# Performance work log

Measured on AMD Instinct MI355X. Metric: run time of the kernel, lower is better.

The kernel has to match this reference:

```python
import jax, jax.numpy as jnp
import numpy as np


def _conv(x, w, pad, groups=1):
    # NCHW conv, OIHW weights, stride 1
    return jax.lax.conv_general_dilated(
        x, w, (1, 1), [(pad, pad), (pad, pad)],
        dimension_numbers=('NCHW', 'OIHW', 'NCHW'),
        feature_group_count=groups)


def setup_inputs() -> dict:
    key = jax.random.key(0)
    ks = jax.random.split(key, 16)
    b, c, h, w = 4, 64, 256, 256
    heads = 8
    s = 0.05
    inp = {
        'x': jax.random.normal(ks[0], (b, c, h, w), jnp.float32),
        # qkv 1x1 conv (with bias) then depthwise 3x3 (with bias)
        'w_qkv': jax.random.normal(ks[1], (3 * c, c, 1, 1), jnp.float32) * s,
        'b_qkv': jax.random.normal(ks[2], (3 * c,), jnp.float32) * s,
        'w_dw': jax.random.normal(ks[3], (3 * c, 1, 3, 3), jnp.float32) * s,
        'b_dw': jax.random.normal(ks[4], (3 * c,), jnp.float32) * s,
        # project_out 1x1 (with bias)
        'w_proj': jax.random.normal(ks[5], (c, c, 1, 1), jnp.float32) * s,
        'b_proj': jax.random.normal(ks[6], (c,), jnp.float32) * s,
        'temperature': jnp.ones((heads, 1, 1), jnp.float32),
        # V_MaskAttention.conv2: 1x1(no bias) -> BN -> 5x5 pad2(no bias)
        'w_m1': jax.random.normal(ks[7], (c, c, 1, 1), jnp.float32) * s,
        'bn_gamma': jnp.ones((c,), jnp.float32),
        'bn_beta': jnp.zeros((c,), jnp.float32),
        'bn_mean': jax.random.normal(ks[8], (c,), jnp.float32) * 0.1,
        'bn_var': jax.random.uniform(ks[9], (c,), jnp.float32, 0.5, 1.5),
        'w_m2': jax.random.normal(ks[10], (c, c, 5, 5), jnp.float32) * s,
    }
    return inp


def reference(x, w_qkv, b_qkv, w_dw, b_dw, w_proj, b_proj, temperature,
              w_m1, bn_gamma, bn_beta, bn_mean, bn_var, w_m2):
    b, c, h, w = x.shape
    heads = temperature.shape[0]

    # qkv conv1x1 + depthwise 3x3 (v chunk computed but unused, as in source)
    qkv = _conv(x, w_qkv, 0) + b_qkv[None, :, None, None]
    qkv = _conv(qkv, w_dw, 1, groups=3 * c) + b_dw[None, :, None, None]
    q, k, _ = jnp.split(qkv, 3, axis=1)

    # V_MaskAttention gated value path (BN in eval mode, eps=1e-5)
    y = _conv(x, w_m1, 0)
    y = (y - bn_mean[None, :, None, None]) * (
        bn_gamma[None, :, None, None]
        / jnp.sqrt(bn_var[None, :, None, None] + 1e-5)) + bn_beta[None, :, None, None]
    x2 = jax.nn.sigmoid(_conv(y, w_m2, 2))
    v = x + x * x2

    def heads_view(t):  # b,(head c),h,w -> b,head,c_head,hw
        return t.reshape(b, heads, c // heads, h * w)

    q = heads_view(q)
    k = heads_view(k)
    v = heads_view(v)

    # L2 normalize over spatial dim (torch F.normalize eps=1e-12)
    q = q / jnp.maximum(jnp.linalg.norm(q, axis=-1, keepdims=True), 1e-12)
    k = k / jnp.maximum(jnp.linalg.norm(k, axis=-1, keepdims=True), 1e-12)

    attn = jnp.einsum('bhcn,bhdn->bhcd', q, k) * temperature[None]  # [b,h,c',c']
    attn = jax.nn.softmax(attn, axis=-1)
    out = jnp.einsum('bhcd,bhdn->bhcn', attn, v).reshape(b, c, h, w)
    return _conv(out, w_proj, 0) + b_proj[None, :, None, None]
```

## Files before the change

kernel.cpp:

```cpp
#include <hip/hip_runtime.h>
#include <math.h>

#define B 4
#define C 64
#define NN 65536

typedef __attribute__((ext_vector_type(8))) short short8;
typedef __attribute__((ext_vector_type(4))) short short4b;
typedef __attribute__((ext_vector_type(4))) float f32x4;
typedef __attribute__((ext_vector_type(4))) unsigned int u32x4;

__device__ inline float bf2f(short s) {
  union { unsigned u; float f; } v; v.u = ((unsigned)(unsigned short)s) << 16; return v.f;
}
__device__ inline short f2bf(float f) {
  union { float f; unsigned u; } v; v.f = f;
  unsigned r = v.u + 0x7FFFu + ((v.u >> 16) & 1u);
  return (short)(r >> 16);
}
__device__ inline float lof(unsigned u) {
  union { unsigned u; float f; } v; v.u = u << 16; return v.f;
}
__device__ inline float hif(unsigned u) {
  union { unsigned u; float f; } v; v.u = u & 0xffff0000u; return v.f;
}

__global__ void k_prep1(const float* __restrict__ wqkv, const float* __restrict__ wm1,
    short* __restrict__ apk, short* __restrict__ apm, float* __restrict__ gram2) {
  for (int idx = blockIdx.x * 256 + threadIdx.x; idx < 20480; idx += 16384) {
    if (idx < 8192) {
      const int j = idx & 7, lane = (idx >> 3) & 63, mt = (idx >> 9) & 7, cc = idx >> 12;
      const int o = mt * 16 + (lane & 15), c = cc * 32 + (lane >> 4) * 8 + j;
      apk[idx] = f2bf(wqkv[o * 64 + c]);
    } else if (idx < 12288) {
      const int k = idx - 8192;
      const int j = k & 7, lane = (k >> 3) & 63, mt = (k >> 9) & 3, cc = k >> 11;
      const int o = mt * 16 + (lane & 15), c = cc * 32 + (lane >> 4) * 8 + j;
      apm[k] = f2bf(wm1[o * 64 + c]);
    } else {
      gram2[idx - 12288] = 0.f;
    }
  }
}

__global__ void k_prep2(const float* __restrict__ w2, short* __restrict__ apw2) {
  for (int idx = blockIdx.x * 256 + threadIdx.x; idx < 25 * 2 * 4 * 64 * 8; idx += 16384) {
    const int j = idx & 7, lane = (idx >> 3) & 63, mt = (idx >> 9) & 3,
              cc = (idx >> 11) & 1, t = idx >> 12;
    const int o = mt * 16 + (lane & 15);
    const int c = cc * 32 + (lane >> 4) * 8 + j;
    apw2[idx] = f2bf(w2[((size_t)o * 64 + c) * 25 + t]);
  }
}

__global__ __launch_bounds__(256) void k_xt(const float* __restrict__ x,
    short* __restrict__ x_t) {
  __shared__ short lds[256 * 72];
  const int b = blockIdx.x >> 8, n0 = (blockIdx.x & 255) << 8;
  const int t = threadIdx.x;
#pragma unroll 4
  for (int c = 0; c < 64; ++c)
    lds[t * 72 + c] = f2bf(x[((size_t)(b * 64 + c)) * NN + n0 + t]);
  __syncthreads();
  short* dst = x_t + ((size_t)(b * NN + n0)) * 64;
#pragma unroll
  for (int it = 0; it < 8; ++it) {
    const int idx = it * 256 + t;
    const int nl = idx >> 3, cb = idx & 7;
    *(short8*)(dst + (size_t)nl * 64 + cb * 8) = *(const short8*)(lds + nl * 72 + cb * 8);
  }
}

__global__ __launch_bounds__(256, 4) void k_qk1x1(const short* __restrict__ x_t,
    const short* __restrict__ apk, const float* __restrict__ bias,
    short* __restrict__ qk) {
  const int b = blockIdx.x >> 10, ntile = blockIdx.x & 1023;
  const int wave = threadIdx.x >> 6, lane = threadIdx.x & 63;
  const int quad = lane >> 4, l15 = lane & 15;
  const int n = ntile * 64 + wave * 16 + l15;
  f32x4 acc[8];
#pragma unroll
  for (int mt = 0; mt < 8; ++mt) acc[mt] = (f32x4){0.f, 0.f, 0.f, 0.f};
#pragma unroll
  for (int cc = 0; cc < 2; ++cc) {
    const short8 bf = *(const short8*)(x_t + ((size_t)(b * NN + n)) * 64 + cc * 32 + quad * 8);
#pragma unroll
    for (int mt = 0; mt < 8; ++mt) {
      const short8 af = *(const short8*)(apk + ((cc * 8 + mt) * 64 + lane) * 8);
      acc[mt] = __builtin_amdgcn_mfma_f32_16x16x32_bf16(af, bf, acc[mt], 0, 0, 0);
    }
  }
#pragma unroll
  for (int mt = 0; mt < 8; ++mt)
#pragma unroll
    for (int reg = 0; reg < 4; ++reg) {
      const int o = mt * 16 + quad * 4 + reg;
      qk[((size_t)(b * 128 + o)) * NN + n] = f2bf(acc[mt][reg] + bias[o]);
    }
}

__global__ __launch_bounds__(256, 3) void k_gram(const short* __restrict__ qk,
    const float* __restrict__ wdw, const float* __restrict__ bdw,
    float* __restrict__ gram2) {
  __shared__ float red[4][256];
  const int bh = blockIdx.x >> 6, chunk = blockIdx.x & 63;
  const int b = bh >> 3, h = bh & 7;
  const int wave = threadIdx.x >> 6, lane = threadIdx.x & 63;
  const int quad = lane >> 4, l15 = lane & 15;
  const int ch = (l15 < 8) ? (h * 8 + l15) : (64 + h * 8 + (l15 - 8));
  const short* plane = qk + ((size_t)(b * 128 + ch)) * NN;
  float wreg[9];
#pragma unroll
  for (int i = 0; i < 9; ++i) wreg[i] = wdw[ch * 9 + i];
  const float bias = bdw[ch];
  const int row = chunk * 4 + wave;
  const short* prow = plane + row * 256;
  u32x4 rb[3][8];
#pragma unroll
  for (int dy = 0; dy < 3; ++dy) {
    if (dy == 0 && row == 0) continue;
    if (dy == 2 && row == 255) continue;
    const short* pr = prow + (dy - 1) * 256 + quad * 8;
#pragma unroll
    for (int s = 0; s < 8; ++s)
      rb[dy][s] = *(const u32x4*)(pr + s * 32);
  }
  f32x4 acc = {0.f, 0.f, 0.f, 0.f};
#pragma unroll
  for (int s = 0; s < 8; ++s) {
    float a[8];
#pragma unroll
    for (int j = 0; j < 8; ++j) a[j] = bias;
#pragma unroll
    for (int dy = 0; dy < 3; ++dy) {
      if (dy == 0 && row == 0) continue;
      if (dy == 2 && row == 255) continue;
      const unsigned w0_ = rb[dy][s][0], w1_ = rb[dy][s][1],
                     w2_ = rb[dy][s][2], w3_ = rb[dy][s][3];
      float m[10];
      m[1] = lof(w0_); m[2] = hif(w0_);
      m[3] = lof(w1_); m[4] = hif(w1_);
      m[5] = lof(w2_); m[6] = hif(w2_);
      m[7] = lof(w3_); m[8] = hif(w3_);
      const unsigned A3 = (unsigned)__shfl((int)w3_, (lane - 16) & 63, 64);
      const unsigned A0 = (unsigned)__shfl((int)w0_, (lane + 16) & 63, 64);
      float m0q0 = 0.f, m9q3 = 0.f;
      if (s > 0) {
        const unsigned B3 = (unsigned)__shfl((int)rb[dy][s - 1][3], (lane + 48) & 63, 64);
        m0q0 = hif(B3);
      }
      if (s < 7) {
        const unsigned B0 = (unsigned)__shfl((int)rb[dy][s + 1][0], (lane - 48) & 63, 64);
        m9q3 = lof(B0);
      }
      m[0] = (quad == 0) ? m0q0 : hif(A3);
      m[9] = (quad == 3) ? m9q3 : lof(A0);
      const float W0 = wreg[dy * 3], W1 = wreg[dy * 3 + 1], W2 = wreg[dy * 3 + 2];
#pragma unroll
      for (int j = 0; j < 8; ++j)
        a[j] = fmaf(W2, m[j + 2], fmaf(W1, m[j + 1], fmaf(W0, m[j], a[j])));
    }
    short8 frag;
#pragma unroll
    for (int j = 0; j < 8; ++j) frag[j] = f2bf(a[j]);
    acc = __builtin_amdgcn_mfma_f32_16x16x32_bf16(frag, frag, acc, 0, 0, 0);
  }
#pragma unroll
  for (int reg = 0; reg < 4; ++reg)
    red[wave][(quad * 4 + reg) * 16 + l15] = acc[reg];
  __syncthreads();
  {
    const int e = threadIdx.x;
    const float s4 = red[0][e] + red[1][e] + red[2][e] + red[3][e];
    atomicAdd(&gram2[bh * 256 + e], s4);
  }
}

__global__ __launch_bounds__(256, 4) void k_m1_bn(const short* __restrict__ x_t,
    const short* __restrict__ apm, const float* __restrict__ gamma,
    const float* __restrict__ beta, const float* __restrict__ mean,
    const float* __restrict__ var, short* __restrict__ y_t) {
  __shared__ short lds[64 * 72];
  const int b = blockIdx.x >> 10, ntile = blockIdx.x & 1023;
  const int wave = threadIdx.x >> 6, lane = threadIdx.x & 63;
  const int quad = lane >> 4, l15 = lane & 15;
  const int n = ntile * 64 + wave * 16 + l15;
  f32x4 acc[4];
#pragma unroll
  for (int mt = 0; mt < 4; ++mt) acc[mt] = (f32x4){0.f, 0.f, 0.f, 0.f};
#pragma unroll
  for (int cc = 0; cc < 2; ++cc) {
    const short8 bf = *(const short8*)(x_t + ((size_t)(b * NN + n)) * 64 + cc * 32 + quad * 8);
#pragma unroll
    for (int mt = 0; mt < 4; ++mt) {
      const short8 af = *(const short8*)(apm + ((cc * 4 + mt) * 64 + lane) * 8);
      acc[mt] = __builtin_amdgcn_mfma_f32_16x16x32_bf16(af, bf, acc[mt], 0, 0, 0);
    }
  }
#pragma unroll
  for (int mt = 0; mt < 4; ++mt)
#pragma unroll
    for (int reg = 0; reg < 4; ++reg) {
      const int o = mt * 16 + quad * 4 + reg;
      const float sc = gamma[o] * rsqrtf(var[o] + 1e-5f);
      lds[(wave * 16 + l15) * 72 + o] = f2bf((acc[mt][reg] - mean[o]) * sc + beta[o]);
    }
  __syncthreads();
  short* dst = y_t + ((size_t)(b * NN + ntile * 64)) * 64;
#pragma unroll
  for (int it = 0; it < 2; ++it) {
    const int idx = it * 256 + threadIdx.x;
    const int lcol = idx >> 3, cb = idx & 7;
    *(short8*)(dst + (size_t)lcol * 64 + cb * 8) = *(const short8*)(lds + lcol * 72 + cb * 8);
  }
}

__global__ __launch_bounds__(256, 2) void k_conv5(const short* __restrict__ y_t,
    const short* __restrict__ apw2, const short* __restrict__ x_t,
    short* __restrict__ v_t) {
  __shared__ short slds[4 * 64 * 76];
  char* sb = (char*)slds;
  const int b = blockIdx.x >> 8;
  const int rg = (blockIdx.x >> 2) & 63, cg = blockIdx.x & 3;
  const int r0 = rg * 4, x0 = cg * 64;
  const int wave = threadIdx.x >> 6, lane = threadIdx.x & 63;
  const int quad = lane >> 4, l15 = lane & 15;
  f32x4 acc[4][4];
#pragma unroll
  for (int mt = 0; mt < 4; ++mt)
#pragma unroll
    for (int nt = 0; nt < 4; ++nt) acc[mt][nt] = (f32x4){0.f, 0.f, 0.f, 0.f};
  for (int cc = 0; cc < 2; ++cc) {
    if (cc) __syncthreads();
    for (int idx = threadIdx.x; idx < 8 * 68 * 4; idx += 256) {
      const int rr = idx / 272, rem = idx - rr * 272;
      const int col = rem >> 2, cb = rem & 3;
      const int gr = r0 - 2 + rr, gc = x0 - 2 + col;
      short8 val = {0, 0, 0, 0, 0, 0, 0, 0};
      if (gr >= 0 && gr < 256 && gc >= 0 && gc < 256)
        val = *(const short8*)(y_t + ((size_t)(b * NN + gr * 256 + gc)) * 64 + cc * 32 + cb * 8);
      const int L = rr * 68 + col;
      *(short8*)(sb + ((L * 64 + cb * 16) ^ (((L >> 1) & 3) << 4))) = val;
    }
    __syncthreads();
    for (int t = 0; t < 25; ++t) {
      const int dy = t / 5 - 2, dx = t % 5 - 2;
      short8 a[4];
#pragma unroll
      for (int mt = 0; mt < 4; ++mt)
        a[mt] = *(const short8*)(apw2 + (((t * 2 + cc) * 4 + mt) * 64 + lane) * 8);
      const int rr = wave + 2 + dy;
#pragma unroll
      for (int nt = 0; nt < 4; ++nt) {
        const int L = rr * 68 + nt * 16 + l15 + 2 + dx;
        const short8 bf =
            *(const short8*)(sb + ((L * 64 + quad * 16) ^ (((L >> 1) & 3) << 4)));
#pragma unroll
        for (int mt = 0; mt < 4; ++mt)
          acc[mt][nt] = __builtin_amdgcn_mfma_f32_16x16x32_bf16(a[mt], bf, acc[mt][nt], 0, 0, 0);
      }
    }
  }
  __syncthreads();
  const int row = r0 + wave;
#pragma unroll
  for (int nt = 0; nt < 4; ++nt) {
    const int lcol = nt * 16 + l15;
    const short* xp = x_t + ((size_t)(b * NN + row * 256 + x0 + lcol)) * 64 + quad * 4;
#pragma unroll
    for (int mt = 0; mt < 4; ++mt) {
      const short4b xv4 = *(const short4b*)(xp + mt * 16);
      short4b pk;
#pragma unroll
      for (int reg = 0; reg < 4; ++reg) {
        const float sg = 1.f / (1.f + __expf(-acc[mt][nt][reg]));
        pk[reg] = f2bf(bf2f(xv4[reg]) * (1.f + sg));
      }
      *(short4b*)(slds + (wave * 64 + lcol) * 76 + mt * 16 + quad * 4) = pk;
    }
  }
  __syncthreads();
#pragma unroll
  for (int it = 0; it < 8; ++it) {
    const int idx = it * 256 + threadIdx.x;
    const int cb = idx & 7, lcol = (idx >> 3) & 63, rr = idx >> 9;
    *(short8*)(v_t + ((size_t)(b * NN + (r0 + rr) * 256 + x0 + lcol)) * 64 + cb * 8) =
        *(const short8*)(slds + (rr * 64 + lcol) * 76 + cb * 8);
  }
}

__global__ __launch_bounds__(256) void k_attn_e(const float* __restrict__ gram2,
    const float* __restrict__ temp, const float* __restrict__ wproj,
    short* __restrict__ Epack) {
  __shared__ float attn[2048];
  const int t = threadIdx.x;
  {
    const int b = t >> 6, h = (t >> 3) & 7, c = t & 7;
    const float* g = gram2 + (b * 8 + h) * 256;
    const float qn = fmaxf(sqrtf(g[c * 16 + c]), 1e-12f);
    const float tp = temp[h];
    float row[8];
    float mx = -1e30f;
#pragma unroll
    for (int d = 0; d < 8; ++d) {
      const float kn = fmaxf(sqrtf(g[(8 + d) * 16 + (8 + d)]), 1e-12f);
      row[d] = g[c * 16 + 8 + d] / (qn * kn) * tp;
      mx = fmaxf(mx, row[d]);
    }
    float s = 0.f;
#pragma unroll
    for (int d = 0; d < 8; ++d) { row[d] = __expf(row[d] - mx); s += row[d]; }
    const float inv = 1.f / s;
#pragma unroll
    for (int d = 0; d < 8; ++d) attn[t * 8 + d] = row[d] * inv;
  }
  __syncthreads();
  for (int idx = t; idx < 16384; idx += 256) {
    const int j = idx & 7, lane = (idx >> 3) & 63, mt = (idx >> 9) & 3,
              cc = (idx >> 11) & 1, b = idx >> 12;
    const int o = mt * 16 + (lane & 15);
    const int cv = cc * 32 + (lane >> 4) * 8 + j;
    const int h = cv >> 3, d = cv & 7;
    float a = 0.f;
#pragma unroll
    for (int c2 = 0; c2 < 8; ++c2)
      a += wproj[o * 64 + h * 8 + c2] * attn[((b * 8 + h) * 8 + c2) * 8 + d];
    Epack[idx] = f2bf(a);
  }
}

__global__ __launch_bounds__(256, 4) void k_out(const short* __restrict__ v_t,
    const short* __restrict__ Epack, const float* __restrict__ bproj,
    float* __restrict__ out) {
  const int b = blockIdx.x >> 10, ntile = blockIdx.x & 1023;
  const int wave = threadIdx.x >> 6, lane = threadIdx.x & 63;
  const int quad = lane >> 4, l15 = lane & 15;
  const int n = ntile * 64 + wave * 16 + l15;
  f32x4 acc[4];
#pragma unroll
  for (int mt = 0; mt < 4; ++mt) acc[mt] = (f32x4){0.f, 0.f, 0.f, 0.f};
#pragma unroll
  for (int cc = 0; cc < 2; ++cc) {
    const short8 bf = *(const short8*)(v_t + ((size_t)(b * NN + n)) * 64 + cc * 32 + quad * 8);
#pragma unroll
    for (int mt = 0; mt < 4; ++mt) {
      const short8 af = *(const short8*)(Epack + (((b * 2 + cc) * 4 + mt) * 64 + lane) * 8);
      acc[mt] = __builtin_amdgcn_mfma_f32_16x16x32_bf16(af, bf, acc[mt], 0, 0, 0);
    }
  }
#pragma unroll
  for (int mt = 0; mt < 4; ++mt)
#pragma unroll
    for (int reg = 0; reg < 4; ++reg) {
      const int o = mt * 16 + quad * 4 + reg;
      out[((size_t)(b * 64 + o)) * NN + n] = acc[mt][reg] + bproj[o];
    }
}

extern "C" void kernel_launch(void* const* d_in, const int* in_sizes, int n_in,
                              void* d_out, int out_size, void* d_ws, size_t ws_size,
                              hipStream_t stream) {
  const float* x     = (const float*)d_in[0];
  const float* wqkv  = (const float*)d_in[1];
  const float* bqkv  = (const float*)d_in[2];
  const float* wdw   = (const float*)d_in[3];
  const float* bdw   = (const float*)d_in[4];
  const float* wproj = (const float*)d_in[5];
  const float* bproj = (const float*)d_in[6];
  const float* temp  = (const float*)d_in[7];
  const float* wm1   = (const float*)d_in[8];
  const float* gamma = (const float*)d_in[9];
  const float* beta  = (const float*)d_in[10];
  const float* mean  = (const float*)d_in[11];
  const float* var   = (const float*)d_in[12];
  const float* wm2   = (const float*)d_in[13];

  char* wsb = (char*)d_ws;
  short* qk    = (short*)(wsb);
  short* v_t   = (short*)(wsb);
  short* apw2  = (short*)(wsb + 33554432);
  short* x_t   = (short*)(wsb + 67108864);
  short* y_t   = (short*)(wsb + 100663296);
  float* gram2 = (float*)(wsb + 134217728);
  short* apk   = (short*)(wsb + 134217728 + 32768);
  short* apm   = (short*)(wsb + 134217728 + 49152);
  short* Epack = (short*)(wsb + 134217728 + 57344);
  float* out   = (float*)d_out;

  k_prep1<<<dim3(64), dim3(256), 0, stream>>>(wqkv, wm1, apk, apm, gram2);
  k_xt<<<dim3(1024), dim3(256), 0, stream>>>(x, x_t);
  k_qk1x1<<<dim3(4096), dim3(256), 0, stream>>>(x_t, apk, bqkv, qk);
  k_gram<<<dim3(2048), dim3(256), 0, stream>>>(qk, wdw, bdw, gram2);
  k_prep2<<<dim3(64), dim3(256), 0, stream>>>(wm2, apw2);
  k_m1_bn<<<dim3(4096), dim3(256), 0, stream>>>(x_t, apm, gamma, beta, mean, var, y_t);
  k_conv5<<<dim3(1024), dim3(256), 0, stream>>>(y_t, apw2, x_t, v_t);
  k_attn_e<<<dim3(1), dim3(256), 0, stream>>>(gram2, temp, wproj, Epack);
  k_out<<<dim3(4096), dim3(256), 0, stream>>>(v_t, Epack, bproj, out);
}
```

Measured before the change: 308.1 us.

## Fold weight prep into main kernels, single-pass conv5 staging, parallelize attn_e

Result: faster. 299.0 us (-3.0%).

```diff
diff --git a/kernel.cpp b/kernel.cpp
--- a/kernel.cpp
+++ b/kernel.cpp
@@ -25,49 +25,41 @@
   union { unsigned u; float f; } v; v.u = u & 0xffff0000u; return v.f;
 }
 
-__global__ void k_prep1(const float* __restrict__ wqkv, const float* __restrict__ wm1,
-    short* __restrict__ apk, short* __restrict__ apm, float* __restrict__ gram2) {
-  for (int idx = blockIdx.x * 256 + threadIdx.x; idx < 20480; idx += 16384) {
-    if (idx < 8192) {
-      const int j = idx & 7, lane = (idx >> 3) & 63, mt = (idx >> 9) & 7, cc = idx >> 12;
-      const int o = mt * 16 + (lane & 15), c = cc * 32 + (lane >> 4) * 8 + j;
-      apk[idx] = f2bf(wqkv[o * 64 + c]);
-    } else if (idx < 12288) {
-      const int k = idx - 8192;
-      const int j = k & 7, lane = (k >> 3) & 63, mt = (k >> 9) & 3, cc = k >> 11;
-      const int o = mt * 16 + (lane & 15), c = cc * 32 + (lane >> 4) * 8 + j;
-      apm[k] = f2bf(wm1[o * 64 + c]);
-    } else {
-      gram2[idx - 12288] = 0.f;
-    }
-  }
-}
-
-__global__ void k_prep2(const float* __restrict__ w2, short* __restrict__ apw2) {
-  for (int idx = blockIdx.x * 256 + threadIdx.x; idx < 25 * 2 * 4 * 64 * 8; idx += 16384) {
-    const int j = idx & 7, lane = (idx >> 3) & 63, mt = (idx >> 9) & 3,
-              cc = (idx >> 11) & 1, t = idx >> 12;
-    const int o = mt * 16 + (lane & 15);
-    const int c = cc * 32 + (lane >> 4) * 8 + j;
-    apw2[idx] = f2bf(w2[((size_t)o * 64 + c) * 25 + t]);
-  }
-}
-
 __global__ __launch_bounds__(256) void k_xt(const float* __restrict__ x,
-    short* __restrict__ x_t) {
-  __shared__ short lds[256 * 72];
+    short* __restrict__ x_t, const float* __restrict__ wqkv,
+    const float* __restrict__ wm1, short* __restrict__ apk,
+    short* __restrict__ apm, float* __restrict__ gram2) {
+  if (blockIdx.x >= 1024) {
+    const int bid = blockIdx.x - 1024;
+    for (int idx = bid * 256 + threadIdx.x; idx < 20480; idx += 16384) {
+      if (idx < 8192) {
+        const int j = idx & 7, lane = (idx >> 3) & 63, mt = (idx >> 9) & 7, cc = idx >> 12;
+        const int o = mt * 16 + (lane & 15), c = cc * 32 + (lane >> 4) * 8 + j;
+        apk[idx] = f2bf(wqkv[o * 64 + c]);
+      } else if (idx < 12288) {
+        const int k = idx - 8192;
+        const int j = k & 7, lane = (k >> 3) & 63, mt = (k >> 9) & 3, cc = k >> 11;
+        const int o = mt * 16 + (lane & 15), c = cc * 32 + (lane >> 4) * 8 + j;
+        apm[k] = f2bf(wm1[o * 64 + c]);
+      } else {
+        gram2[idx - 12288] = 0.f;
+      }
+    }
+    return;
+  }
+  __shared__ short lds[256 * 66];
   const int b = blockIdx.x >> 8, n0 = (blockIdx.x & 255) << 8;
   const int t = threadIdx.x;
 #pragma unroll 4
   for (int c = 0; c < 64; ++c)
-    lds[t * 72 + c] = f2bf(x[((size_t)(b * 64 + c)) * NN + n0 + t]);
+    lds[t * 66 + c] = f2bf(x[((size_t)(b * 64 + c)) * NN + n0 + t]);
   __syncthreads();
   short* dst = x_t + ((size_t)(b * NN + n0)) * 64;
 #pragma unroll
   for (int it = 0; it < 8; ++it) {
     const int idx = it * 256 + t;
     const int nl = idx >> 3, cb = idx & 7;
-    *(short8*)(dst + (size_t)nl * 64 + cb * 8) = *(const short8*)(lds + nl * 72 + cb * 8);
+    *(short8*)(dst + (size_t)nl * 64 + cb * 8) = *(const short8*)(lds + nl * 66 + cb * 8);
   }
 }
 
@@ -179,8 +171,20 @@
 __global__ __launch_bounds__(256, 4) void k_m1_bn(const short* __restrict__ x_t,
     const short* __restrict__ apm, const float* __restrict__ gamma,
     const float* __restrict__ beta, const float* __restrict__ mean,
-    const float* __restrict__ var, short* __restrict__ y_t) {
-  __shared__ short lds[64 * 72];
+    const float* __restrict__ var, short* __restrict__ y_t,
+    const float* __restrict__ w2, short* __restrict__ apw2) {
+  if (blockIdx.x >= 4096) {
+    const int bid = blockIdx.x - 4096;
+    for (int idx = bid * 256 + threadIdx.x; idx < 25 * 2 * 4 * 64 * 8; idx += 16384) {
+      const int j = idx & 7, lane = (idx >> 3) & 63, mt = (idx >> 9) & 3,
+                cc = (idx >> 11) & 1, t = idx >> 12;
+      const int o = mt * 16 + (lane & 15);
+      const int c = cc * 32 + (lane >> 4) * 8 + j;
+      apw2[idx] = f2bf(w2[((size_t)o * 64 + c) * 25 + t]);
+    }
+    return;
+  }
+  __shared__ short lds[64 * 66];
   const int b = blockIdx.x >> 10, ntile = blockIdx.x & 1023;
   const int wave = threadIdx.x >> 6, lane = threadIdx.x & 63;
   const int quad = lane >> 4, l15 = lane & 15;
@@ -203,7 +207,7 @@
     for (int reg = 0; reg < 4; ++reg) {
       const int o = mt * 16 + quad * 4 + reg;
       const float sc = gamma[o] * rsqrtf(var[o] + 1e-5f);
-      lds[(wave * 16 + l15) * 72 + o] = f2bf((acc[mt][reg] - mean[o]) * sc + beta[o]);
+      lds[(wave * 16 + l15) * 66 + o] = f2bf((acc[mt][reg] - mean[o]) * sc + beta[o]);
     }
   __syncthreads();
   short* dst = y_t + ((size_t)(b * NN + ntile * 64)) * 64;
@@ -211,14 +215,14 @@
   for (int it = 0; it < 2; ++it) {
     const int idx = it * 256 + threadIdx.x;
     const int lcol = idx >> 3, cb = idx & 7;
-    *(short8*)(dst + (size_t)lcol * 64 + cb * 8) = *(const short8*)(lds + lcol * 72 + cb * 8);
+    *(short8*)(dst + (size_t)lcol * 64 + cb * 8) = *(const short8*)(lds + lcol * 66 + cb * 8);
   }
 }
 
 __global__ __launch_bounds__(256, 2) void k_conv5(const short* __restrict__ y_t,
     const short* __restrict__ apw2, const short* __restrict__ x_t,
     short* __restrict__ v_t) {
-  __shared__ short slds[4 * 64 * 76];
+  __shared__ short slds[8 * 68 * 64];
   char* sb = (char*)slds;
   const int b = blockIdx.x >> 8;
   const int rg = (blockIdx.x >> 2) & 63, cg = blockIdx.x & 3;
@@ -230,34 +234,36 @@
   for (int mt = 0; mt < 4; ++mt)
 #pragma unroll
     for (int nt = 0; nt < 4; ++nt) acc[mt][nt] = (f32x4){0.f, 0.f, 0.f, 0.f};
-  for (int cc = 0; cc < 2; ++cc) {
-    if (cc) __syncthreads();
-    for (int idx = threadIdx.x; idx < 8 * 68 * 4; idx += 256) {
-      const int rr = idx / 272, rem = idx - rr * 272;
-      const int col = rem >> 2, cb = rem & 3;
-      const int gr = r0 - 2 + rr, gc = x0 - 2 + col;
-      short8 val = {0, 0, 0, 0, 0, 0, 0, 0};
-      if (gr >= 0 && gr < 256 && gc >= 0 && gc < 256)
-        val = *(const short8*)(y_t + ((size_t)(b * NN + gr * 256 + gc)) * 64 + cc * 32 + cb * 8);
-      const int L = rr * 68 + col;
-      *(short8*)(sb + ((L * 64 + cb * 16) ^ (((L >> 1) & 3) << 4))) = val;
-    }
-    __syncthreads();
-    for (int t = 0; t < 25; ++t) {
-      const int dy = t / 5 - 2, dx = t % 5 - 2;
-      short8 a[4];
-#pragma unroll
-      for (int mt = 0; mt < 4; ++mt)
-        a[mt] = *(const short8*)(apw2 + (((t * 2 + cc) * 4 + mt) * 64 + lane) * 8);
-      const int rr = wave + 2 + dy;
-#pragma unroll
-      for (int nt = 0; nt < 4; ++nt) {
-        const int L = rr * 68 + nt * 16 + l15 + 2 + dx;
-        const short8 bf =
-            *(const short8*)(sb + ((L * 64 + quad * 16) ^ (((L >> 1) & 3) << 4)));
-#pragma unroll
-        for (int mt = 0; mt < 4; ++mt)
-          acc[mt][nt] = __builtin_amdgcn_mfma_f32_16x16x32_bf16(a[mt], bf, acc[mt][nt], 0, 0, 0);
+  for (int idx = threadIdx.x; idx < 8 * 68 * 8; idx += 256) {
+    const int rr = idx / 544, rem = idx - rr * 544;
+    const int col = rem >> 3, cb = rem & 7;
+    const int gr = r0 - 2 + rr, gc = x0 - 2 + col;
+    short8 val = {0, 0, 0, 0, 0, 0, 0, 0};
+    if (gr >= 0 && gr < 256 && gc >= 0 && gc < 256)
+      val = *(const short8*)(y_t + ((size_t)(b * NN + gr * 256 + gc)) * 64 + cb * 8);
+    const int L = rr * 68 + col;
+    *(short8*)(sb + L * 128 + ((cb * 16) ^ ((L & 7) << 4))) = val;
+  }
+  __syncthreads();
+  for (int t = 0; t < 25; ++t) {
+    const int dy = t / 5 - 2, dx = t % 5 - 2;
+    short8 a0[4], a1[4];
+#pragma unroll
+    for (int mt = 0; mt < 4; ++mt) {
+      a0[mt] = *(const short8*)(apw2 + (((t * 2 + 0) * 4 + mt) * 64 + lane) * 8);
+      a1[mt] = *(const short8*)(apw2 + (((t * 2 + 1) * 4 + mt) * 64 + lane) * 8);
+    }
+    const int rr = wave + 2 + dy;
+#pragma unroll
+    for (int nt = 0; nt < 4; ++nt) {
+      const int L = rr * 68 + nt * 16 + l15 + 2 + dx;
+      const int off0 = L * 128 + ((quad * 16) ^ ((L & 7) << 4));
+      const short8 bf0 = *(const short8*)(sb + off0);
+      const short8 bf1 = *(const short8*)(sb + (off0 ^ 64));
+#pragma unroll
+      for (int mt = 0; mt < 4; ++mt) {
+        acc[mt][nt] = __builtin_amdgcn_mfma_f32_16x16x32_bf16(a0[mt], bf0, acc[mt][nt], 0, 0, 0);
+        acc[mt][nt] = __builtin_amdgcn_mfma_f32_16x16x32_bf16(a1[mt], bf1, acc[mt][nt], 0, 0, 0);
       }
     }
   }
@@ -315,7 +321,7 @@
     for (int d = 0; d < 8; ++d) attn[t * 8 + d] = row[d] * inv;
   }
   __syncthreads();
-  for (int idx = t; idx < 16384; idx += 256) {
+  for (int idx = blockIdx.x * 1024 + t; idx < (blockIdx.x + 1) * 1024; idx += 256) {
     const int j = idx & 7, lane = (idx >> 3) & 63, mt = (idx >> 9) & 3,
               cc = (idx >> 11) & 1, b = idx >> 12;
     const int o = mt * 16 + (lane & 15);
@@ -387,13 +393,12 @@
   short* Epack = (short*)(wsb + 134217728 + 57344);
   float* out   = (float*)d_out;
 
-  k_prep1<<<dim3(64), dim3(256), 0, stream>>>(wqkv, wm1, apk, apm, gram2);
-  k_xt<<<dim3(1024), dim3(256), 0, stream>>>(x, x_t);
+  k_xt<<<dim3(1088), dim3(256), 0, stream>>>(x, x_t, wqkv, wm1, apk, apm, gram2);
   k_qk1x1<<<dim3(4096), dim3(256), 0, stream>>>(x_t, apk, bqkv, qk);
   k_gram<<<dim3(2048), dim3(256), 0, stream>>>(qk, wdw, bdw, gram2);
-  k_prep2<<<dim3(64), dim3(256), 0, stream>>>(wm2, apw2);
-  k_m1_bn<<<dim3(4096), dim3(256), 0, stream>>>(x_t, apm, gamma, beta, mean, var, y_t);
+  k_m1_bn<<<dim3(4160), dim3(256), 0, stream>>>(x_t, apm, gamma, beta, mean, var, y_t,
+                                                wm2, apw2);
   k_conv5<<<dim3(1024), dim3(256), 0, stream>>>(y_t, apw2, x_t, v_t);
-  k_attn_e<<<dim3(1), dim3(256), 0, stream>>>(gram2, temp, wproj, Epack);
+  k_attn_e<<<dim3(16), dim3(256), 0, stream>>>(gram2, temp, wproj, Epack);
   k_out<<<dim3(4096), dim3(256), 0, stream>>>(v_t, Epack, bproj, out);
 }
```
